# Kernel tuning notes

Measured on AMD Instinct MI355X. Metric: run time of the kernel, lower is better.

## Reference

```python
import jax, jax.numpy as jnp
import numpy as np

B, S, D, H, L = 8, 1024, 512, 8, 6
DK = D // H
DFF = 4 * D
EPS = 1e-5
SCALE = float(np.sqrt(DK))  # torch: sqrt(d_k)


def setup_inputs() -> dict:
    key = jax.random.key(0)
    ks = jax.random.split(key, 10)
    init = lambda k, shape: jax.random.normal(k, shape, jnp.float32) * 0.02
    return {
        "x": jax.random.normal(ks[0], (B, S, D), jnp.float32),
        "qkv_w": init(ks[1], (L, D, 3 * D)),
        "qkv_b": init(ks[2], (L, 3 * D)),
        "out_w": init(ks[3], (L, D, D)),
        "out_b": init(ks[4], (L, D)),
        "ln1_g": jnp.ones((L, D), jnp.float32),
        "ln1_b": jnp.zeros((L, D), jnp.float32),
        "mlp_w1": init(ks[5], (L, D, DFF)),
        "mlp_b1": init(ks[6], (L, DFF)),
        "mlp_w2": init(ks[7], (L, DFF, D)),
        "mlp_b2": init(ks[8], (L, D)),
        "ln2_g": jnp.ones((L, D), jnp.float32),
        "ln2_b": jnp.zeros((L, D), jnp.float32),
    }


def _layer_norm(x, g, b):
    m = jnp.mean(x, axis=-1, keepdims=True)
    v = jnp.var(x, axis=-1, keepdims=True)  # biased var, matches torch LayerNorm
    return (x - m) * jax.lax.rsqrt(v + EPS) * g + b


def reference(x, qkv_w, qkv_b, out_w, out_b, ln1_g, ln1_b,
              mlp_w1, mlp_b1, mlp_w2, mlp_b2, ln2_g, ln2_b):
    b, s, d = x.shape
    causal = jnp.tril(jnp.ones((s, s), dtype=bool))  # [S,S]
    for i in range(L):
        # --- causal self-attention, post-LN residual (dropout = eval identity) ---
        qkv = x @ qkv_w[i] + qkv_b[i]                      # [B,S,3D]
        q, k, v = jnp.split(qkv, 3, axis=-1)
        q = q.reshape(b, s, H, DK)
        k = k.reshape(b, s, H, DK)
        v = v.reshape(b, s, H, DK)
        att = jnp.einsum('bqhd,bkhd->bhqk', q, k) / SCALE  # [B,H,S,S]
        att = jnp.where(causal, att, -jnp.inf)
        att = jax.nn.softmax(att, axis=-1)
        o = jnp.einsum('bhqk,bkhd->bqhd', att, v).reshape(b, s, d)
        x = _layer_norm(o @ out_w[i] + out_b[i] + x, ln1_g[i], ln1_b[i])
        # --- MLP, post-LN residual ---
        h = jax.nn.relu(x @ mlp_w1[i] + mlp_b1[i]) @ mlp_w2[i] + mlp_b2[i]
        x = _layer_norm(x + h, ln2_g[i], ln2_b[i])
    return x
```

## Files before the change

kernel.cpp:

```cpp
#include <hip/hip_runtime.h>
#include <math.h>

#define Bn   8
#define Sn   1024
#define Dn   512
#define Hn   8
#define DKn  64
#define Ln   6
#define DFFn 2048
#define Mn   (Bn * Sn)

typedef __bf16 bf16x8 __attribute__((ext_vector_type(8)));
typedef __bf16 bf16x4 __attribute__((ext_vector_type(4)));
typedef __bf16 bf16x2 __attribute__((ext_vector_type(2)));
typedef float  f32x4  __attribute__((ext_vector_type(4)));

__device__ __forceinline__ void gl_lds16(const void* g, void* l) {
    __builtin_amdgcn_global_load_lds(
        (const __attribute__((address_space(1))) void*)g,
        (__attribute__((address_space(3))) void*)l, 16, 0, 0);
}

__global__ __launch_bounds__(256) void k_cast_bf16(const float* __restrict__ in,
                                                   __bf16* __restrict__ out, int n) {
    int i = blockIdx.x * 256 + threadIdx.x;
    if (i < n) out[i] = (__bf16)in[i];
}

__global__ __launch_bounds__(256) void k_cast_f32(const __bf16* __restrict__ in,
                                                  float* __restrict__ out, int n) {
    int i = (blockIdx.x * 256 + threadIdx.x) * 4;
    if (i < n) {
        bf16x4 v = *(const bf16x4*)&in[i];
        f32x4 o = {(float)v[0], (float)v[1], (float)v[2], (float)v[3]};
        *(f32x4*)&out[i] = o;
    }
}

__global__ __launch_bounds__(256) void k_trans_all(
    const float* __restrict__ qkv_w, const float* __restrict__ out_w,
    const float* __restrict__ w1, const float* __restrict__ w2,
    __bf16* __restrict__ Wq, __bf16* __restrict__ Wo,
    __bf16* __restrict__ W1o, __bf16* __restrict__ W2o)
{
    const int t = blockIdx.x;
    const float* src; __bf16* dst; int K, N, n0, k0;
    if (t < 768)       { src = qkv_w; dst = Wq;  K = 512;  N = 1536; int u = t;        n0 = (u % 48) * 32; k0 = (u / 48) * 32; }
    else if (t < 1024) { src = out_w; dst = Wo;  K = 512;  N = 512;  int u = t - 768;  n0 = (u % 16) * 32; k0 = (u / 16) * 32; }
    else if (t < 2048) { src = w1;    dst = W1o; K = 512;  N = 2048; int u = t - 1024; n0 = (u % 64) * 32; k0 = (u / 64) * 32; }
    else               { src = w2;    dst = W2o; K = 2048; N = 512;  int u = t - 2048; n0 = (u % 16) * 32; k0 = (u / 16) * 32; }

    __shared__ float tt[32][33];
    const int tx = threadIdx.x, ty = threadIdx.y;
    #pragma unroll
    for (int r = 0; r < 4; r++)
        tt[ty + 8 * r][tx] = src[(size_t)(k0 + ty + 8 * r) * N + n0 + tx];
    __syncthreads();
    #pragma unroll
    for (int r = 0; r < 4; r++)
        dst[(size_t)(n0 + ty + 8 * r) * K + k0 + tx] = (__bf16)tt[tx][ty + 8 * r];
}

template <int RELU, int OUTBF, int JT, int VW>
__global__ __launch_bounds__(256) void k_gemm_mfma(
    const __bf16* __restrict__ A, const __bf16* __restrict__ Bt,
    const float* __restrict__ bias, void* __restrict__ Cout,
    __bf16* __restrict__ Vt, int M, int N, int K, int NBX)
{
    constexpr int BN = JT * 32;
    __shared__ __bf16 As[128][64];
    __shared__ __bf16 Bs[BN][64];
    const int tid  = threadIdx.x;
    const int lane = tid & 63;
    const int wave = tid >> 6;
    const int wy   = wave >> 1, wx = wave & 1;
    const int m16  = lane & 15, quad = lane >> 4;

    const int cpx = gridDim.x >> 3;
    const int id  = (blockIdx.x & 7) * cpx + (blockIdx.x >> 3);
    const int bm  = (id / NBX) * 128;
    const int bn  = (id % NBX) * BN;

    f32x4 acc[4][JT];
    #pragma unroll
    for (int i = 0; i < 4; i++)
        #pragma unroll
        for (int j = 0; j < JT; j++)
            acc[i][j] = (f32x4){0.f, 0.f, 0.f, 0.f};

    const __bf16* Ap = A  + (size_t)bm * K;
    const __bf16* Bp = Bt + (size_t)bn * K;

    const int sw0 = ((quad    ) ^ (m16 & 7)) * 8;
    const int sw1 = ((quad + 4) ^ (m16 & 7)) * 8;

    for (int k0 = 0; k0 < K; k0 += 64) {
        __syncthreads();
        #pragma unroll
        for (int c = 0; c < 4; c++) {
            int lin = tid + c * 256;
            int row = lin >> 3, uu = lin & 7;
            int su  = (uu ^ (row & 7)) << 3;
            gl_lds16(Ap + (size_t)row * K + k0 + su, (void*)(&As[0][0] + lin * 8));
        }
        #pragma unroll
        for (int c = 0; c < JT; c++) {
            int lin = tid + c * 256;
            int row = lin >> 3, uu = lin & 7;
            int su  = (uu ^ (row & 7)) << 3;
            gl_lds16(Bp + (size_t)row * K + k0 + su, (void*)(&Bs[0][0] + lin * 8));
        }
        __syncthreads();

        bf16x8 af[4][2], bfr[JT][2];
        #pragma unroll
        for (int i = 0; i < 4; i++) {
            af[i][0] = *(const bf16x8*)&As[wy * 64 + i * 16 + m16][sw0];
            af[i][1] = *(const bf16x8*)&As[wy * 64 + i * 16 + m16][sw1];
        }
        #pragma unroll
        for (int j = 0; j < JT; j++) {
            bfr[j][0] = *(const bf16x8*)&Bs[wx * JT * 16 + j * 16 + m16][sw0];
            bfr[j][1] = *(const bf16x8*)&Bs[wx * JT * 16 + j * 16 + m16][sw1];
        }
        #pragma unroll
        for (int hc = 0; hc < 2; hc++)
            #pragma unroll
            for (int i = 0; i < 4; i++)
                #pragma unroll
                for (int j = 0; j < JT; j++)
                    acc[i][j] = __builtin_amdgcn_mfma_f32_16x16x32_bf16(
                        af[i][hc], bfr[j][hc], acc[i][j], 0, 0, 0);
    }

    float*  Cf = (float*)Cout;
    __bf16* Cb = (__bf16*)Cout;
    #pragma unroll
    for (int i = 0; i < 4; i++) {
        const int row0 = bm + wy * 64 + i * 16 + quad * 4;
        #pragma unroll
        for (int j = 0; j < JT; j++) {
            const int col = bn + wx * JT * 16 + j * 16 + m16;
            const float bv = bias[col];
            float vv[4];
            #pragma unroll
            for (int r = 0; r < 4; r++) {
                float v = acc[i][j][r] + bv;
                if (RELU) v = fmaxf(v, 0.f);
                vv[r] = v;
                if (OUTBF) Cb[(size_t)(row0 + r) * N + col] = (__bf16)v;
                else       Cf[(size_t)(row0 + r) * N + col] = v;
            }
            if (VW && col >= 1024) {
                const int cc = col - 1024;
                const int bb = row0 >> 10, ss = row0 & 1023;
                bf16x4 pv;
                #pragma unroll
                for (int r = 0; r < 4; r++) pv[r] = (__bf16)vv[r];
                *(bf16x4*)&Vt[((size_t)(bb * Hn + (cc >> 6)) * DKn + (cc & 63)) * Sn + ss] = pv;
            }
        }
    }
}

__device__ __forceinline__ void softmax_update(
    f32x4 sv[4], float m[4], float l[4], f32x4 acc[4],
    bool diag, int wave16, int quad, int m16,
    __bf16 (*Pw)[72], bf16x8& pf0, bf16x8& pf1)
{
    #pragma unroll
    for (int j = 0; j < 4; j++)
        #pragma unroll
        for (int r = 0; r < 4; r++) {
            float v = sv[j][r] * 0.125f;
            if (diag && (j * 16 + m16) > (wave16 + quad * 4 + r)) v = -1e30f;
            sv[j][r] = v;
        }

    float pm[4];
    #pragma unroll
    for (int r = 0; r < 4; r++)
        pm[r] = fmaxf(fmaxf(sv[0][r], sv[1][r]), fmaxf(sv[2][r], sv[3][r]));
    #pragma unroll
    for (int off = 1; off < 16; off <<= 1)
        #pragma unroll
        for (int r = 0; r < 4; r++)
            pm[r] = fmaxf(pm[r], __shfl_xor(pm[r], off, 16));

    bool grew = false;
    #pragma unroll
    for (int r = 0; r < 4; r++) grew = grew || (pm[r] > m[r] + 8.f);
    if (__any((int)grew)) {
        #pragma unroll
        for (int r = 0; r < 4; r++) {
            float mn = fmaxf(m[r], pm[r]);
            float al = __expf(m[r] - mn);
            m[r] = mn;
            l[r] *= al;
            #pragma unroll
            for (int j = 0; j < 4; j++) acc[j][r] *= al;
        }
    }

    float rs[4] = {0.f, 0.f, 0.f, 0.f};
    #pragma unroll
    for (int j = 0; j < 4; j++)
        #pragma unroll
        for (int r = 0; r < 4; r++) {
            float p = __expf(sv[j][r] - m[r]);
            rs[r] += p;
            Pw[quad * 4 + r][j * 16 + m16] = (__bf16)p;
        }
    #pragma unroll
    for (int off = 1; off < 16; off <<= 1)
        #pragma unroll
        for (int r = 0; r < 4; r++)
            rs[r] += __shfl_xor(rs[r], off, 16);
    #pragma unroll
    for (int r = 0; r < 4; r++) l[r] += rs[r];

    pf0 = *(const bf16x8*)&Pw[m16][quad * 8];
    pf1 = *(const bf16x8*)&Pw[m16][32 + quad * 8];
}

__global__ __launch_bounds__(512, 4) void k_attn_mfma(
    const __bf16* __restrict__ qkv, const __bf16* __restrict__ Vt,
    __bf16* __restrict__ o)
{
    const int id = blockIdx.x;
    const int pr = id >> 6;
    const int b  = (id >> 3) & 7;
    const int h  = id & 7;
    const int tid  = threadIdx.x;
    const int lane = tid & 63, wave = tid >> 6;
    const int m16  = lane & 15, quad = lane >> 4;
    const int isB  = wave >> 2;
    const int wave16 = (wave & 3) * 16;
    const int qtA  = pr, qtB = 15 - pr;
    const int qt   = isB ? qtB : qtA;

    __shared__ __bf16 Kb[2][64][64];
    __shared__ __bf16 Vb[2][64][64];
    __shared__ __bf16 Ps[8][16][72];

    const __bf16* base = qkv + (size_t)b * Sn * 1536 + h * DKn;
    const __bf16* vtb  = Vt + (size_t)(b * Hn + h) * DKn * Sn;
    __bf16 (*Pw)[72] = Ps[wave];

    const int sw0 = ((quad    ) ^ (m16 & 7)) * 8;
    const int sw1 = ((quad + 4) ^ (m16 & 7)) * 8;

    const int srow = tid >> 3;
    const int ssu  = ((tid & 7) ^ (srow & 7)) * 8;

    #define STAGE(KT, BB)                                                       \
        {                                                                       \
            gl_lds16(base + (size_t)((KT) * 64 + srow) * 1536 + 512 + ssu,      \
                     (void*)(&Kb[BB][0][0] + tid * 8));                         \
            gl_lds16(vtb + (size_t)srow * Sn + (KT) * 64 + ssu,                 \
                     (void*)(&Vb[BB][0][0] + tid * 8));                         \
        }

    STAGE(0, 0);

    bf16x8 q0, q1;
    {
        const __bf16* qa = base + (size_t)(qt * 64 + wave16 + m16) * 1536 + quad * 8;
        q0 = *(const bf16x8*)qa; q1 = *(const bf16x8*)(qa + 32);
    }

    float m[4], l[4];
    f32x4 acc[4];
    #pragma unroll
    for (int r = 0; r < 4; r++) {
        m[r] = -1e30f; l[r] = 0.f;
        acc[r] = (f32x4){0.f, 0.f, 0.f, 0.f};
    }

    __syncthreads();

    for (int kt = 0; kt <= qtB; kt++) {
        const int buf = kt & 1;
        if (kt < qtB) STAGE(kt + 1, buf ^ 1);

        if (isB || kt <= qtA) {
            f32x4 sv[4];
            __builtin_amdgcn_s_setprio(1);
            #pragma unroll
            for (int j = 0; j < 4; j++) {
                const int rk = j * 16 + m16;
                bf16x8 kf0 = *(const bf16x8*)&Kb[buf][rk][sw0];
                bf16x8 kf1 = *(const bf16x8*)&Kb[buf][rk][sw1];
                f32x4 s = (f32x4){0.f, 0.f, 0.f, 0.f};
                s = __builtin_amdgcn_mfma_f32_16x16x32_bf16(q0, kf0, s, 0, 0, 0);
                s = __builtin_amdgcn_mfma_f32_16x16x32_bf16(q1, kf1, s, 0, 0, 0);
                sv[j] = s;
            }
            __builtin_amdgcn_s_setprio(0);

            bf16x8 vf[4][2];
            #pragma unroll
            for (int jd = 0; jd < 4; jd++) {
                const int rv = jd * 16 + m16;
                vf[jd][0] = *(const bf16x8*)&Vb[buf][rv][sw0];
                vf[jd][1] = *(const bf16x8*)&Vb[buf][rv][sw1];
            }

            bf16x8 p0, p1;
            softmax_update(sv, m, l, acc, kt == qt, wave16, quad, m16, Pw, p0, p1);

            __builtin_amdgcn_s_setprio(1);
            #pragma unroll
            for (int jd = 0; jd < 4; jd++) {
                acc[jd] = __builtin_amdgcn_mfma_f32_16x16x32_bf16(p0, vf[jd][0], acc[jd], 0, 0, 0);
                acc[jd] = __builtin_amdgcn_mfma_f32_16x16x32_bf16(p1, vf[jd][1], acc[jd], 0, 0, 0);
            }
            __builtin_amdgcn_s_setprio(0);
        }

        __syncthreads();
    }
    #undef STAGE

    #pragma unroll
    for (int r = 0; r < 4; r++) l[r] = 1.0f / l[r];
    #pragma unroll
    for (int jd = 0; jd < 4; jd++)
        #pragma unroll
        for (int r = 0; r < 4; r++) {
            const int row = b * Sn + qt * 64 + wave16 + quad * 4 + r;
            o[(size_t)row * Dn + h * DKn + jd * 16 + m16] = (__bf16)(acc[jd][r] * l[r]);
        }
}

__device__ inline float block_reduce_sum(float v, float* red, int tid) {
    red[tid] = v;
    __syncthreads();
    for (int s = 128; s > 0; s >>= 1) {
        if (tid < s) red[tid] += red[tid + s];
        __syncthreads();
    }
    float r = red[0];
    __syncthreads();
    return r;
}

__global__ __launch_bounds__(256) void k_residual_ln(
    const __bf16* __restrict__ t, __bf16* __restrict__ xb,
    const float* __restrict__ g, const float* __restrict__ be)
{
    __shared__ float red[256];
    const int row = blockIdx.x, tid = threadIdx.x;
    const size_t base = (size_t)row * Dn + tid * 2;

    bf16x2 tv = *(const bf16x2*)&t[base];
    bf16x2 xv = *(const bf16x2*)&xb[base];
    float v0 = (float)tv[0] + (float)xv[0];
    float v1 = (float)tv[1] + (float)xv[1];

    float mean = block_reduce_sum(v0 + v1, red, tid) * (1.0f / Dn);
    float d0 = v0 - mean, d1 = v1 - mean;
    float var = block_reduce_sum(d0 * d0 + d1 * d1, red, tid) * (1.0f / Dn);
    float inv = rsqrtf(var + 1e-5f);

    const float2 gv = *(const float2*)&g[tid * 2];
    const float2 bv = *(const float2*)&be[tid * 2];
    bf16x2 ov;
    ov[0] = (__bf16)(d0 * inv * gv.x + bv.x);
    ov[1] = (__bf16)(d1 * inv * gv.y + bv.y);
    *(bf16x2*)&xb[base] = ov;
}

extern "C" void kernel_launch(void* const* d_in, const int* in_sizes, int n_in,
                              void* d_out, int out_size, void* d_ws, size_t ws_size,
                              hipStream_t stream)
{
    const float* x_in   = (const float*)d_in[0];
    const float* qkv_w  = (const float*)d_in[1];
    const float* qkv_b  = (const float*)d_in[2];
    const float* out_w  = (const float*)d_in[3];
    const float* out_b  = (const float*)d_in[4];
    const float* ln1_g  = (const float*)d_in[5];
    const float* ln1_b  = (const float*)d_in[6];
    const float* mlp_w1 = (const float*)d_in[7];
    const float* mlp_b1 = (const float*)d_in[8];
    const float* mlp_w2 = (const float*)d_in[9];
    const float* mlp_b2 = (const float*)d_in[10];
    const float* ln2_g  = (const float*)d_in[11];
    const float* ln2_b  = (const float*)d_in[12];

    char* p = (char*)d_ws;
    __bf16* Xb   = (__bf16*)p; p += (size_t)Mn * Dn * 2;
    __bf16* QKVb = (__bf16*)p; p += (size_t)Mn * 3 * Dn * 2;
    __bf16* AOb  = (__bf16*)p; p += (size_t)Mn * Dn * 2;
    __bf16* Hb   = (__bf16*)p; p += (size_t)Mn * DFFn * 2;
    __bf16* Wq   = (__bf16*)p; p += (size_t)3 * Dn * Dn * 2;
    __bf16* Wo   = (__bf16*)p; p += (size_t)Dn * Dn * 2;
    __bf16* W1   = (__bf16*)p; p += (size_t)DFFn * Dn * 2;
    __bf16* W2   = (__bf16*)p; p += (size_t)Dn * DFFn * 2;
    __bf16* Vt   = Hb;
    __bf16* BUF3b = (__bf16*)d_out;

    k_cast_bf16<<<(Mn * Dn) / 256, 256, 0, stream>>>(x_in, Xb, Mn * Dn);

    for (int l = 0; l < Ln; l++) {
        k_trans_all<<<3072, dim3(32, 8), 0, stream>>>(
            qkv_w + (size_t)l * Dn * 3 * Dn, out_w + (size_t)l * Dn * Dn,
            mlp_w1 + (size_t)l * Dn * DFFn, mlp_w2 + (size_t)l * DFFn * Dn,
            Wq, Wo, W1, W2);

        k_gemm_mfma<0, 1, 4, 1><<<768, 256, 0, stream>>>(
            Xb, Wq, qkv_b + (size_t)l * 3 * Dn, QKVb, Vt, Mn, 3 * Dn, Dn, 12);
        k_attn_mfma<<<512, 512, 0, stream>>>(QKVb, Vt, AOb);
        k_gemm_mfma<0, 1, 2, 0><<<512, 256, 0, stream>>>(
            AOb, Wo, out_b + (size_t)l * Dn, BUF3b, nullptr, Mn, Dn, Dn, 8);
        k_residual_ln<<<Mn, 256, 0, stream>>>(BUF3b, Xb,
            ln1_g + (size_t)l * Dn, ln1_b + (size_t)l * Dn);
        k_gemm_mfma<1, 1, 4, 0><<<1024, 256, 0, stream>>>(
            Xb, W1, mlp_b1 + (size_t)l * DFFn, Hb, nullptr, Mn, DFFn, Dn, 16);
        k_gemm_mfma<0, 1, 2, 0><<<512, 256, 0, stream>>>(
            Hb, W2, mlp_b2 + (size_t)l * Dn, BUF3b, nullptr, Mn, Dn, DFFn, 8);
        k_residual_ln<<<Mn, 256, 0, stream>>>(BUF3b, Xb,
            ln2_g + (size_t)l * Dn, ln2_b + (size_t)l * Dn);
    }

    k_cast_f32<<<(Mn * Dn) / 1024, 256, 0, stream>>>(Xb, (float*)d_out, Mn * Dn);
}
```

Before: 1.043 ms.

## Use wave-per-row LayerNorm, batch weight transposes, fuse final fp32 cast

Rewrites the residual LayerNorm so each 64-lane wave handles one row with 8-element vector loads and shuffle reductions, instead of a 256-thread block doing shared-memory tree reductions. Weights for all layers are now transposed to bf16 in one launch up front rather than once per layer. The final LayerNorm writes fp32 directly, which removes the separate cast kernel. In exchange, workspace grows to hold every layer's bf16 weights, and BUF3b moves from the output buffer into the workspace.

Measured after the change: 956.1 us. 8.3% less time.

```diff
diff --git a/kernel.cpp b/kernel.cpp
--- a/kernel.cpp
+++ b/kernel.cpp
@@ -27,28 +27,23 @@
     if (i < n) out[i] = (__bf16)in[i];
 }
 
-__global__ __launch_bounds__(256) void k_cast_f32(const __bf16* __restrict__ in,
-                                                  float* __restrict__ out, int n) {
-    int i = (blockIdx.x * 256 + threadIdx.x) * 4;
-    if (i < n) {
-        bf16x4 v = *(const bf16x4*)&in[i];
-        f32x4 o = {(float)v[0], (float)v[1], (float)v[2], (float)v[3]};
-        *(f32x4*)&out[i] = o;
-    }
-}
-
 __global__ __launch_bounds__(256) void k_trans_all(
     const float* __restrict__ qkv_w, const float* __restrict__ out_w,
     const float* __restrict__ w1, const float* __restrict__ w2,
     __bf16* __restrict__ Wq, __bf16* __restrict__ Wo,
     __bf16* __restrict__ W1o, __bf16* __restrict__ W2o)
 {
-    const int t = blockIdx.x;
+    const int lay = blockIdx.x / 3072;
+    const int t   = blockIdx.x % 3072;
     const float* src; __bf16* dst; int K, N, n0, k0;
-    if (t < 768)       { src = qkv_w; dst = Wq;  K = 512;  N = 1536; int u = t;        n0 = (u % 48) * 32; k0 = (u / 48) * 32; }
-    else if (t < 1024) { src = out_w; dst = Wo;  K = 512;  N = 512;  int u = t - 768;  n0 = (u % 16) * 32; k0 = (u / 16) * 32; }
-    else if (t < 2048) { src = w1;    dst = W1o; K = 512;  N = 2048; int u = t - 1024; n0 = (u % 64) * 32; k0 = (u / 64) * 32; }
-    else               { src = w2;    dst = W2o; K = 2048; N = 512;  int u = t - 2048; n0 = (u % 16) * 32; k0 = (u / 16) * 32; }
+    if (t < 768)       { src = qkv_w + (size_t)lay * Dn * 3 * Dn; dst = Wq  + (size_t)lay * 3 * Dn * Dn;
+                         K = 512;  N = 1536; int u = t;        n0 = (u % 48) * 32; k0 = (u / 48) * 32; }
+    else if (t < 1024) { src = out_w + (size_t)lay * Dn * Dn;     dst = Wo  + (size_t)lay * Dn * Dn;
+                         K = 512;  N = 512;  int u = t - 768;  n0 = (u % 16) * 32; k0 = (u / 16) * 32; }
+    else if (t < 2048) { src = w1 + (size_t)lay * Dn * DFFn;      dst = W1o + (size_t)lay * DFFn * Dn;
+                         K = 512;  N = 2048; int u = t - 1024; n0 = (u % 64) * 32; k0 = (u / 64) * 32; }
+    else               { src = w2 + (size_t)lay * DFFn * Dn;      dst = W2o + (size_t)lay * Dn * DFFn;
+                         K = 2048; N = 512;  int u = t - 2048; n0 = (u % 16) * 32; k0 = (u / 16) * 32; }
 
     __shared__ float tt[32][33];
     const int tx = threadIdx.x, ty = threadIdx.y;
@@ -333,42 +328,62 @@
         }
 }
 
-__device__ inline float block_reduce_sum(float v, float* red, int tid) {
-    red[tid] = v;
-    __syncthreads();
-    for (int s = 128; s > 0; s >>= 1) {
-        if (tid < s) red[tid] += red[tid + s];
-        __syncthreads();
-    }
-    float r = red[0];
-    __syncthreads();
-    return r;
-}
-
+template <int FINAL>
 __global__ __launch_bounds__(256) void k_residual_ln(
     const __bf16* __restrict__ t, __bf16* __restrict__ xb,
-    const float* __restrict__ g, const float* __restrict__ be)
-{
-    __shared__ float red[256];
-    const int row = blockIdx.x, tid = threadIdx.x;
-    const size_t base = (size_t)row * Dn + tid * 2;
-
-    bf16x2 tv = *(const bf16x2*)&t[base];
-    bf16x2 xv = *(const bf16x2*)&xb[base];
-    float v0 = (float)tv[0] + (float)xv[0];
-    float v1 = (float)tv[1] + (float)xv[1];
-
-    float mean = block_reduce_sum(v0 + v1, red, tid) * (1.0f / Dn);
-    float d0 = v0 - mean, d1 = v1 - mean;
-    float var = block_reduce_sum(d0 * d0 + d1 * d1, red, tid) * (1.0f / Dn);
-    float inv = rsqrtf(var + 1e-5f);
-
-    const float2 gv = *(const float2*)&g[tid * 2];
-    const float2 bv = *(const float2*)&be[tid * 2];
-    bf16x2 ov;
-    ov[0] = (__bf16)(d0 * inv * gv.x + bv.x);
-    ov[1] = (__bf16)(d1 * inv * gv.y + bv.y);
-    *(bf16x2*)&xb[base] = ov;
+    const float* __restrict__ g, const float* __restrict__ be,
+    float* __restrict__ outf)
+{
+    const int row  = (blockIdx.x << 2) | (threadIdx.x >> 6);
+    const int lane = threadIdx.x & 63;
+    const size_t base = (size_t)row * Dn + lane * 8;
+
+    bf16x8 tv = *(const bf16x8*)&t[base];
+    bf16x8 xv = *(const bf16x8*)&xb[base];
+    float v[8];
+    float s = 0.f;
+    #pragma unroll
+    for (int i = 0; i < 8; i++) {
+        v[i] = (float)tv[i] + (float)xv[i];
+        s += v[i];
+    }
+    #pragma unroll
+    for (int off = 1; off < 64; off <<= 1) s += __shfl_xor(s, off);
+    const float mean = s * (1.0f / Dn);
+
+    float vs = 0.f;
+    #pragma unroll
+    for (int i = 0; i < 8; i++) {
+        v[i] -= mean;
+        vs += v[i] * v[i];
+    }
+    #pragma unroll
+    for (int off = 1; off < 64; off <<= 1) vs += __shfl_xor(vs, off);
+    const float inv = rsqrtf(vs * (1.0f / Dn) + 1e-5f);
+
+    const f32x4 g0 = *(const f32x4*)&g[lane * 8];
+    const f32x4 g1 = *(const f32x4*)&g[lane * 8 + 4];
+    const f32x4 b0 = *(const f32x4*)&be[lane * 8];
+    const f32x4 b1 = *(const f32x4*)&be[lane * 8 + 4];
+
+    if (FINAL) {
+        f32x4 o0, o1;
+        #pragma unroll
+        for (int i = 0; i < 4; i++) {
+            o0[i] = v[i] * inv * g0[i] + b0[i];
+            o1[i] = v[i + 4] * inv * g1[i] + b1[i];
+        }
+        *(f32x4*)&outf[base]     = o0;
+        *(f32x4*)&outf[base + 4] = o1;
+    } else {
+        bf16x8 ov;
+        #pragma unroll
+        for (int i = 0; i < 4; i++) {
+            ov[i]     = (__bf16)(v[i] * inv * g0[i] + b0[i]);
+            ov[i + 4] = (__bf16)(v[i + 4] * inv * g1[i] + b1[i]);
+        }
+        *(bf16x8*)&xb[base] = ov;
+    }
 }
 
 extern "C" void kernel_launch(void* const* d_in, const int* in_sizes, int n_in,
@@ -390,39 +405,44 @@
     const float* ln2_b  = (const float*)d_in[12];
 
     char* p = (char*)d_ws;
-    __bf16* Xb   = (__bf16*)p; p += (size_t)Mn * Dn * 2;
-    __bf16* QKVb = (__bf16*)p; p += (size_t)Mn * 3 * Dn * 2;
-    __bf16* AOb  = (__bf16*)p; p += (size_t)Mn * Dn * 2;
-    __bf16* Hb   = (__bf16*)p; p += (size_t)Mn * DFFn * 2;
-    __bf16* Wq   = (__bf16*)p; p += (size_t)3 * Dn * Dn * 2;
-    __bf16* Wo   = (__bf16*)p; p += (size_t)Dn * Dn * 2;
-    __bf16* W1   = (__bf16*)p; p += (size_t)DFFn * Dn * 2;
-    __bf16* W2   = (__bf16*)p; p += (size_t)Dn * DFFn * 2;
-    __bf16* Vt   = Hb;
-    __bf16* BUF3b = (__bf16*)d_out;
+    __bf16* Xb    = (__bf16*)p; p += (size_t)Mn * Dn * 2;
+    __bf16* QKVb  = (__bf16*)p; p += (size_t)Mn * 3 * Dn * 2;
+    __bf16* AOb   = (__bf16*)p; p += (size_t)Mn * Dn * 2;
+    __bf16* Hb    = (__bf16*)p; p += (size_t)Mn * DFFn * 2;
+    __bf16* BUF3b = (__bf16*)p; p += (size_t)Mn * Dn * 2;
+    __bf16* Wq    = (__bf16*)p; p += (size_t)Ln * 3 * Dn * Dn * 2;
+    __bf16* Wo    = (__bf16*)p; p += (size_t)Ln * Dn * Dn * 2;
+    __bf16* W1    = (__bf16*)p; p += (size_t)Ln * DFFn * Dn * 2;
+    __bf16* W2    = (__bf16*)p; p += (size_t)Ln * Dn * DFFn * 2;
+    __bf16* Vt    = Hb;
 
     k_cast_bf16<<<(Mn * Dn) / 256, 256, 0, stream>>>(x_in, Xb, Mn * Dn);
 
+    k_trans_all<<<Ln * 3072, dim3(32, 8), 0, stream>>>(
+        qkv_w, out_w, mlp_w1, mlp_w2, Wq, Wo, W1, W2);
+
     for (int l = 0; l < Ln; l++) {
-        k_trans_all<<<3072, dim3(32, 8), 0, stream>>>(
-            qkv_w + (size_t)l * Dn * 3 * Dn, out_w + (size_t)l * Dn * Dn,
-            mlp_w1 + (size_t)l * Dn * DFFn, mlp_w2 + (size_t)l * DFFn * Dn,
-            Wq, Wo, W1, W2);
+        const __bf16* Wql = Wq + (size_t)l * 3 * Dn * Dn;
+        const __bf16* Wol = Wo + (size_t)l * Dn * Dn;
+        const __bf16* W1l = W1 + (size_t)l * DFFn * Dn;
+        const __bf16* W2l = W2 + (size_t)l * Dn * DFFn;
 
         k_gemm_mfma<0, 1, 4, 1><<<768, 256, 0, stream>>>(
-            Xb, Wq, qkv_b + (size_t)l * 3 * Dn, QKVb, Vt, Mn, 3 * Dn, Dn, 12);
+            Xb, Wql, qkv_b + (size_t)l * 3 * Dn, QKVb, Vt, Mn, 3 * Dn, Dn, 12);
         k_attn_mfma<<<512, 512, 0, stream>>>(QKVb, Vt, AOb);
         k_gemm_mfma<0, 1, 2, 0><<<512, 256, 0, stream>>>(
-            AOb, Wo, out_b + (size_t)l * Dn, BUF3b, nullptr, Mn, Dn, Dn, 8);
-        k_residual_ln<<<Mn, 256, 0, stream>>>(BUF3b, Xb,
-            ln1_g + (size_t)l * Dn, ln1_b + (size_t)l * Dn);
+            AOb, Wol, out_b + (size_t)l * Dn, BUF3b, nullptr, Mn, Dn, Dn, 8);
+        k_residual_ln<0><<<Mn / 4, 256, 0, stream>>>(BUF3b, Xb,
+            ln1_g + (size_t)l * Dn, ln1_b + (size_t)l * Dn, nullptr);
         k_gemm_mfma<1, 1, 4, 0><<<1024, 256, 0, stream>>>(
-            Xb, W1, mlp_b1 + (size_t)l * DFFn, Hb, nullptr, Mn, DFFn, Dn, 16);
+            Xb, W1l, mlp_b1 + (size_t)l * DFFn, Hb, nullptr, Mn, DFFn, Dn, 16);
         k_gemm_mfma<0, 1, 2, 0><<<512, 256, 0, stream>>>(
-            Hb, W2, mlp_b2 + (size_t)l * Dn, BUF3b, nullptr, Mn, Dn, DFFn, 8);
-        k_residual_ln<<<Mn, 256, 0, stream>>>(BUF3b, Xb,
-            ln2_g + (size_t)l * Dn, ln2_b + (size_t)l * Dn);
-    }
-
-    k_cast_f32<<<(Mn * Dn) / 1024, 256, 0, stream>>>(Xb, (float*)d_out, Mn * Dn);
-}
+            Hb, W2l, mlp_b2 + (size_t)l * Dn, BUF3b, nullptr, Mn, Dn, DFFn, 8);
+        if (l == Ln - 1)
+            k_residual_ln<1><<<Mn / 4, 256, 0, stream>>>(BUF3b, Xb,
+                ln2_g + (size_t)l * Dn, ln2_b + (size_t)l * Dn, (float*)d_out);
+        else
+            k_residual_ln<0><<<Mn / 4, 256, 0, stream>>>(BUF3b, Xb,
+                ln2_g + (size_t)l * Dn, ln2_b + (size_t)l * Dn, nullptr);
+    }
+}
```
